# Kernel tuning notes

Measured on AMD Instinct MI355X. Metric: run time of the kernel, lower is better.

Reference implementation:

```python
import jax, jax.numpy as jnp
import numpy as np

B, T, D = 4, 2048, 1024
E, K, H = 8, 2, 2048

def setup_inputs() -> dict:
    key = jax.random.key(0)
    ks = jax.random.split(key, 5)
    scale = 0.02
    x = jax.random.normal(ks[0], (B, T, D), dtype=jnp.float32)
    gate_w = jax.random.normal(ks[1], (E, D), dtype=jnp.float32) * scale   # Linear(D->E) weight [out,in]
    w_gate = jax.random.normal(ks[2], (E, H, D), dtype=jnp.float32) * scale
    w_in = jax.random.normal(ks[3], (E, H, D), dtype=jnp.float32) * scale
    w_out = jax.random.normal(ks[4], (E, D, H), dtype=jnp.float32) * scale
    return {"x": x, "gate_w": gate_w, "w_gate": w_gate, "w_in": w_in, "w_out": w_out}

def reference(x, gate_w, w_gate, w_in, w_out):
    # Router: logits (B,T,E) -> top-k -> softmax over the k selected logits
    logits = jnp.einsum('btd,ed->bte', x, gate_w)
    topk_vals, topk_idx = jax.lax.top_k(logits, K)          # (B,T,K)
    routing = jax.nn.softmax(topk_vals, axis=-1)            # (B,T,K)

    out = jnp.zeros_like(x)
    # Masked-matmul: loop over the small fixed expert bank (E=8)
    for e in range(E):
        sel = (topk_idx == e)                               # (B,T,K) bool
        mask = sel.any(axis=-1)                             # (B,T)
        w = jnp.sum(routing * sel.astype(routing.dtype), axis=-1)  # (B,T)
        mx = x * mask[..., None].astype(x.dtype)            # (B,T,D)
        h = jax.nn.silu(jnp.einsum('btd,hd->bth', mx, w_gate[e])) * jnp.einsum('btd,hd->bth', mx, w_in[e])
        out = out + jnp.einsum('bth,dh->btd', h, w_out[e]) * w[..., None]
    return out
```

## Files before the change

kernel.cpp:

```cpp
#include <hip/hip_runtime.h>
#include <stdint.h>
#include <stddef.h>

#define NTOK 8192
#define DDIM 1024
#define NEXP 8
#define HDIM 2048
#define LSTRIDE (NTOK + 256)
#define NCHUNK 128
#define MAXROWS (2 * NTOK + NEXP * 256)

typedef __attribute__((ext_vector_type(4))) float f32x4;
typedef __attribute__((ext_vector_type(8))) short s16x8;
typedef __attribute__((ext_vector_type(4))) short s16x4;

static __device__ __forceinline__ unsigned short f2bf(float f) {
  union { float f; unsigned u; } v; v.f = f;
  unsigned r = v.u + 0x7FFFu + ((v.u >> 16) & 1u);
  return (unsigned short)(r >> 16);
}
static __device__ __forceinline__ float bf2f(unsigned short h) {
  union { unsigned u; float f; } v; v.u = ((unsigned)h) << 16;
  return v.f;
}

static __device__ __forceinline__ void gll16(const void* g, void* l) {
  __builtin_amdgcn_global_load_lds((const __attribute__((address_space(1))) void*)g,
                                   (__attribute__((address_space(3))) void*)l, 16, 0, 0);
}

#define BAR_MID() __builtin_amdgcn_s_barrier()
#define BAR_END() do { __builtin_amdgcn_s_barrier(); __builtin_amdgcn_sched_barrier(0); } while (0)
#define LGKM0() do { asm volatile("s_waitcnt lgkmcnt(0)" ::: "memory"); __builtin_amdgcn_sched_barrier(0); } while (0)
#define VMW6() asm volatile("s_waitcnt vmcnt(6)" ::: "memory")
#define VMW0() asm volatile("s_waitcnt vmcnt(0)" ::: "memory")

__global__ void k_sentinel(float* out) { if (threadIdx.x == 0) out[0] = 1.0e6f; }

__global__ __launch_bounds__(256) void k_prep(const float* __restrict__ x,
    const float* __restrict__ gw,
    const float* __restrict__ wgate, const float* __restrict__ win, const float* __restrict__ wout,
    unsigned short* __restrict__ wgb, unsigned short* __restrict__ wib, unsigned short* __restrict__ wob,
    unsigned* __restrict__ tokE, float2* __restrict__ tokW2, unsigned short* __restrict__ xbf) {
  int b = blockIdx.x;
  if (b >= 2048) {
    const float* srcs[3] = { wgate, win, wout };
    unsigned short* dsts[3] = { wgb, wib, wob };
    int g = (b - 2048) * 256 + threadIdx.x;
    const int stride = 1536 * 256;
#pragma unroll
    for (int it = 0; it < 16; ++it) {
      int arr = g >> 21;
      int idx = g & ((1 << 21) - 1);
      const f32x4* s = (const f32x4*)(srcs[arr] + (size_t)idx * 8);
      f32x4 a = s[0], c = s[1];
      s16x8 o;
      o[0] = f2bf(a[0]); o[1] = f2bf(a[1]); o[2] = f2bf(a[2]); o[3] = f2bf(a[3]);
      o[4] = f2bf(c[0]); o[5] = f2bf(c[1]); o[6] = f2bf(c[2]); o[7] = f2bf(c[3]);
      *(s16x8*)(dsts[arr] + (size_t)idx * 8) = o;
      g += stride;
    }
    return;
  }
  int lane = threadIdx.x & 63;
  int t = b * 4 + (threadIdx.x >> 6);
  const f32x4* x4 = (const f32x4*)x;
  const f32x4* g4 = (const f32x4*)gw;
  f32x4 xr[4];
#pragma unroll
  for (int j = 0; j < 4; ++j) xr[j] = x4[(size_t)t * 256 + j * 64 + lane];
#pragma unroll
  for (int j = 0; j < 4; ++j) {
    s16x4 o;
    o[0] = f2bf(xr[j][0]); o[1] = f2bf(xr[j][1]); o[2] = f2bf(xr[j][2]); o[3] = f2bf(xr[j][3]);
    *(s16x4*)(xbf + (size_t)t * DDIM + (j * 64 + lane) * 4) = o;
  }
  float le[8];
#pragma unroll
  for (int e = 0; e < 8; ++e) {
    float p = 0.f;
#pragma unroll
    for (int j = 0; j < 4; ++j) {
      f32x4 g = g4[e * 256 + j * 64 + lane];
      p += xr[j][0] * g[0] + xr[j][1] * g[1] + xr[j][2] * g[2] + xr[j][3] * g[3];
    }
#pragma unroll
    for (int off = 32; off > 0; off >>= 1) p += __shfl_xor(p, off, 64);
    le[e] = p;
  }
  if (lane == 0) {
    int i0 = 0; float v0 = le[0];
#pragma unroll
    for (int e = 1; e < 8; ++e) if (le[e] > v0) { v0 = le[e]; i0 = e; }
    int i1 = -1; float v1 = 0.f;
#pragma unroll
    for (int e = 0; e < 8; ++e) if (e != i0 && (i1 < 0 || le[e] > v1)) { v1 = le[e]; i1 = e; }
    float bb = __expf(v1 - v0);
    float s = 1.f + bb;
    tokE[t] = (unsigned)i0 | ((unsigned)i1 << 8);
    tokW2[t] = make_float2(1.f / s, bb / s);
  }
}

__global__ __launch_bounds__(64) void k_hist(const unsigned* __restrict__ tokE,
                                             int* __restrict__ cntTable) {
  __shared__ int c8[NEXP];
  int tid = threadIdx.x, c = blockIdx.x;
  if (tid < NEXP) c8[tid] = 0;
  __syncthreads();
  unsigned v = tokE[c * 64 + tid];
  atomicAdd(&c8[v & 255], 1);
  atomicAdd(&c8[(v >> 8) & 255], 1);
  __syncthreads();
  if (tid < NEXP) cntTable[tid * NCHUNK + c] = c8[tid];
}

__global__ __launch_bounds__(64) void k_scan(const int* __restrict__ cntTable,
                                             int* __restrict__ ctrl, int* __restrict__ cbL) {
  __shared__ int tot[NEXP];
  int e = threadIdx.x;
  if (e < NEXP) {
    int s = 0;
    for (int c = 0; c < NCHUNK; ++c) s += cntTable[e * NCHUNK + c];
    tot[e] = s; ctrl[e] = s;
  }
  __syncthreads();
  if (e == 0) {
    int acc = 0;
    for (int q = 0; q < NEXP; ++q) { ctrl[8 + q] = acc; acc += (tot[q] + 255) & ~255; }
  }
  if (e < NEXP) {
    int run = 0;
    for (int c = 0; c < NCHUNK; ++c) { cbL[e * NCHUNK + c] = run; run += cntTable[e * NCHUNK + c]; }
  }
}

__global__ __launch_bounds__(64) void k_scatter(const unsigned* __restrict__ tokE,
    const float2* __restrict__ tokW2, const int* __restrict__ cbL,
    int* __restrict__ listTok, float* __restrict__ listW, int* __restrict__ listSlot) {
  __shared__ int lcnt[NEXP];
  int tid = threadIdx.x, c = blockIdx.x;
  if (tid < NEXP) lcnt[tid] = 0;
  __syncthreads();
  int t = c * 64 + tid;
  unsigned v = tokE[t];
  int e0 = v & 255, e1 = (v >> 8) & 255;
  float2 w = tokW2[t];
  int l0 = atomicAdd(&lcnt[e0], 1);
  int l1 = atomicAdd(&lcnt[e1], 1);
  int i0 = cbL[e0 * NCHUNK + c] + l0;
  int i1 = cbL[e1 * NCHUNK + c] + l1;
  listTok[e0 * LSTRIDE + i0] = t; listW[e0 * LSTRIDE + i0] = w.x; listSlot[e0 * LSTRIDE + i0] = 0;
  listTok[e1 * LSTRIDE + i1] = t; listW[e1 * LSTRIDE + i1] = w.y; listSlot[e1 * LSTRIDE + i1] = 1;
}

__global__ __launch_bounds__(512, 2) void k_gemm1(const unsigned short* __restrict__ xbf,
    const unsigned short* __restrict__ wg, const unsigned short* __restrict__ wi,
    const int* __restrict__ ctrl, const int* __restrict__ listTok,
    unsigned short* __restrict__ hbuf) {
  int e = blockIdx.z;
  int cnt = ctrl[e];
  int m0 = blockIdx.y * 256;
  if (m0 >= cnt) return;
  int rowb = ctrl[8 + e];
  int n0 = blockIdx.x * 128;

  __shared__ __align__(16) char lds[131072];
  char* ldsc = &lds[0];

  int tid = threadIdx.x, lane = tid & 63, wv = tid >> 6;
  int wm = wv >> 1, wn = wv & 1;

  int srow = tid >> 3;
  int scol = (((tid & 7) ^ ((tid >> 3) & 7)) << 4);
  int sdst = wv << 10;
  const char* pA[2][2];
  const char* pBg[2];
  const char* pBi[2];
#pragma unroll
  for (int rg = 0; rg < 2; ++rg)
#pragma unroll
    for (int sb = 0; sb < 2; ++sb) {
      int tok = listTok[e * LSTRIDE + m0 + rg * 128 + sb * 64 + srow];
      pA[rg][sb] = (const char*)xbf + (size_t)tok * 2048 + scol;
    }
#pragma unroll
  for (int sb = 0; sb < 2; ++sb) {
    pBg[sb] = (const char*)wg + ((size_t)e * HDIM + n0 + sb * 64 + srow) * 2048 + scol;
    pBi[sb] = (const char*)wi + ((size_t)e * HDIM + n0 + sb * 64 + srow) * 2048 + scol;
  }

  int rowB = (lane & 15) << 7;
  int mk = (lane & 7) << 4;
  int q16 = (lane >> 4) << 4;
  int c0 = q16 ^ mk, c1 = (q16 + 64) ^ mk;
  int aO0 = 32768 + (wm >> 1) * 16384 + ((wm & 1) * 64) * 128 + rowB + c0;
  int aO1 = aO0 - c0 + c1;
  int gO0 = (wn * 64) * 128 + rowB + c0;
  int gO1 = gO0 - c0 + c1;
  int iO0 = 16384 + (wn * 64) * 128 + rowB + c0;
  int iO1 = iO0 - c0 + c1;

#define G1_STA(BUF, RG, KO) do { \
    gll16(pA[RG][0] + (KO), ldsc + (BUF) + 32768 + (RG) * 16384 + sdst); \
    gll16(pA[RG][1] + (KO), ldsc + (BUF) + 32768 + (RG) * 16384 + 8192 + sdst); } while (0)
#define G1_STG(BUF, KO) do { \
    gll16(pBg[0] + (KO), ldsc + (BUF) + sdst); \
    gll16(pBg[1] + (KO), ldsc + (BUF) + 8192 + sdst); } while (0)
#define G1_STI(BUF, KO) do { \
    gll16(pBi[0] + (KO), ldsc + (BUF) + 16384 + sdst); \
    gll16(pBi[1] + (KO), ldsc + (BUF) + 16384 + 8192 + sdst); } while (0)
#define G1_RDA(BUF) { _Pragma("unroll") for (int mf = 0; mf < 4; ++mf) { \
    af[mf][0] = *(const s16x8*)(ldsc + (BUF) + aO0 + mf * 2048); \
    af[mf][1] = *(const s16x8*)(ldsc + (BUF) + aO1 + mf * 2048); } }
#define G1_RDG(BUF) { _Pragma("unroll") for (int nf = 0; nf < 4; ++nf) { \
    bg[nf][0] = *(const s16x8*)(ldsc + (BUF) + gO0 + nf * 2048); \
    bg[nf][1] = *(const s16x8*)(ldsc + (BUF) + gO1 + nf * 2048); } }
#define G1_RDI(BUF) { _Pragma("unroll") for (int nf = 0; nf < 4; ++nf) { \
    bi[nf][0] = *(const s16x8*)(ldsc + (BUF) + iO0 + nf * 2048); \
    bi[nf][1] = *(const s16x8*)(ldsc + (BUF) + iO1 + nf * 2048); } }
#define G1_MMG(NH) do { __builtin_amdgcn_s_setprio(1); \
    _Pragma("unroll") for (int mf = 0; mf < 4; ++mf) _Pragma("unroll") for (int nf = 0; nf < 2; ++nf) { \
      accg[mf][(NH)*2+nf] = __builtin_amdgcn_mfma_f32_16x16x32_bf16(af[mf][0], bg[(NH)*2+nf][0], accg[mf][(NH)*2+nf], 0, 0, 0); \
      accg[mf][(NH)*2+nf] = __builtin_amdgcn_mfma_f32_16x16x32_bf16(af[mf][1], bg[(NH)*2+nf][1], accg[mf][(NH)*2+nf], 0, 0, 0); } \
    __builtin_amdgcn_s_setprio(0); } while (0)
#define G1_MMI(NH) do { __builtin_amdgcn_s_setprio(1); \
    _Pragma("unroll") for (int mf = 0; mf < 4; ++mf) _Pragma("unroll") for (int nf = 0; nf < 2; ++nf) { \
      acci[mf][(NH)*2+nf] = __builtin_amdgcn_mfma_f32_16x16x32_bf16(af[mf][0], bi[(NH)*2+nf][0], acci[mf][(NH)*2+nf], 0, 0, 0); \
      acci[mf][(NH)*2+nf] = __builtin_amdgcn_mfma_f32_16x16x32_bf16(af[mf][1], bi[(NH)*2+nf][1], acci[mf][(NH)*2+nf], 0, 0, 0); } \
    __builtin_amdgcn_s_setprio(0); } while (0)

  f32x4 accg[4][4], acci[4][4];
#pragma unroll
  for (int a = 0; a < 4; ++a)
#pragma unroll
    for (int b = 0; b < 4; ++b) { accg[a][b] = (f32x4){0.f,0.f,0.f,0.f}; acci[a][b] = (f32x4){0.f,0.f,0.f,0.f}; }
  s16x8 af[4][2], bg[4][2], bi[4][2];

  G1_STG(0, 0); G1_STA(0, 0, 0); G1_STI(0, 0); G1_STA(0, 1, 0);
  G1_STG(65536, 128); G1_STA(65536, 0, 128); G1_STI(65536, 128);
  VMW6();
  BAR_END();

  const int NIT = DDIM / 128;
  for (int i = 0; i < NIT; ++i) {
    const int koC = (2 * i + 1) * 128, koA = (2 * i + 2) * 128, koB = (2 * i + 3) * 128;
    const bool more = (i + 1 < NIT);
    G1_RDA(0); G1_RDG(0);
    G1_STA(65536, 1, koC);
    BAR_MID(); LGKM0();
    G1_MMG(0);
    BAR_END();
    if (more) G1_STG(0, koA);
    BAR_MID();
    G1_MMG(1);
    BAR_END();
    G1_RDI(0);
    if (more) G1_STA(0, 0, koA);
    BAR_MID(); LGKM0();
    G1_MMI(0);
    BAR_END();
    if (more) G1_STI(0, koA);
    BAR_MID();
    G1_MMI(1);
    if (more) VMW6(); else VMW0();
    BAR_END();
    G1_RDA(65536); G1_RDG(65536);
    if (more) G1_STA(0, 1, koA);
    BAR_MID(); LGKM0();
    G1_MMG(0);
    BAR_END();
    if (more) G1_STG(65536, koB);
    BAR_MID();
    G1_MMG(1);
    BAR_END();
    G1_RDI(65536);
    if (more) G1_STA(65536, 0, koB);
    BAR_MID(); LGKM0();
    G1_MMI(0);
    BAR_END();
    if (more) G1_STI(65536, koB);
    BAR_MID();
    G1_MMI(1);
    if (more) VMW6();
    BAR_END();
  }

#pragma unroll
  for (int mf = 0; mf < 4; ++mf)
#pragma unroll
    for (int j = 0; j < 4; ++j) {
      int r = wm * 64 + mf * 16 + ((lane >> 4) << 2) + j;
      size_t rowoff = (size_t)(rowb + m0 + r) * HDIM;
#pragma unroll
      for (int nf = 0; nf < 4; ++nf) {
        int cc = n0 + wn * 64 + nf * 16 + (lane & 15);
        float g = accg[mf][nf][j];
        float iv = acci[mf][nf][j];
        float hv = g / (1.f + __expf(-g)) * iv;
        hbuf[rowoff + cc] = f2bf(hv);
      }
    }
#undef G1_STA
#undef G1_STG
#undef G1_STI
#undef G1_RDA
#undef G1_RDG
#undef G1_RDI
#undef G1_MMG
#undef G1_MMI
}

__global__ __launch_bounds__(512, 2) void k_gemm2(const unsigned short* __restrict__ hbuf,
    const unsigned short* __restrict__ wo, const int* __restrict__ ctrl,
    const int* __restrict__ listTok, const float* __restrict__ listW,
    const int* __restrict__ listSlot, unsigned short* __restrict__ ybuf) {
  int e = blockIdx.z;
  int cnt = ctrl[e];
  int m0 = blockIdx.y * 256;
  if (m0 >= cnt) return;
  int rowb = ctrl[8 + e];
  int n0 = blockIdx.x * 128;

  __shared__ __align__(16) char lds[98304];
  char* ldsc = &lds[0];
#define BUF2 49152

  int tid = threadIdx.x, lane = tid & 63, wv = tid >> 6;
  int wm = wv >> 1, wn = wv & 1;

  int srow = tid >> 3;
  int scol = (((tid & 7) ^ ((tid >> 3) & 7)) << 4);
  int sdst = wv << 10;
  const char* pA[2][2];
  const char* pB[2];
#pragma unroll
  for (int rg = 0; rg < 2; ++rg)
#pragma unroll
    for (int sb = 0; sb < 2; ++sb)
      pA[rg][sb] = (const char*)hbuf + (size_t)(rowb + m0 + rg * 128 + sb * 64 + srow) * 4096 + scol;
#pragma unroll
  for (int sb = 0; sb < 2; ++sb)
    pB[sb] = (const char*)wo + ((size_t)e * DDIM + n0 + sb * 64 + srow) * 4096 + scol;

  int rowB = (lane & 15) << 7;
  int mk = (lane & 7) << 4;
  int q16 = (lane >> 4) << 4;
  int c0 = q16 ^ mk, c1 = (q16 + 64) ^ mk;
  int aO0 = wm * 8192 + rowB + c0;
  int aO1 = aO0 - c0 + c1;
  int bO0 = 32768 + wn * 8192 + rowB + c0;
  int bO1 = bO0 - c0 + c1;

#define G2_STA(BUF, RG, KO) do { \
    gll16(pA[RG][0] + (KO), ldsc + (BUF) + (RG) * 16384 + sdst); \
    gll16(pA[RG][1] + (KO), ldsc + (BUF) + (RG) * 16384 + 8192 + sdst); } while (0)
#define G2_STB(BUF, KO) do { \
    gll16(pB[0] + (KO), ldsc + (BUF) + 32768 + sdst); \
    gll16(pB[1] + (KO), ldsc + (BUF) + 32768 + 8192 + sdst); } while (0)
#define G2_RDA(BUF) { _Pragma("unroll") for (int mf = 0; mf < 4; ++mf) { \
    af[mf][0] = *(const s16x8*)(ldsc + (BUF) + aO0 + mf * 2048); \
    af[mf][1] = *(const s16x8*)(ldsc + (BUF) + aO1 + mf * 2048); } }
#define G2_RDB(BUF) { _Pragma("unroll") for (int nf = 0; nf < 4; ++nf) { \
    bf[nf][0] = *(const s16x8*)(ldsc + (BUF) + bO0 + nf * 2048); \
    bf[nf][1] = *(const s16x8*)(ldsc + (BUF) + bO1 + nf * 2048); } }
#define G2_MM(NH) do { __builtin_amdgcn_s_setprio(1); \
    _Pragma("unroll") for (int mf = 0; mf < 4; ++mf) _Pragma("unroll") for (int nf = 0; nf < 2; ++nf) { \
      acc[mf][(NH)*2+nf] = __builtin_amdgcn_mfma_f32_16x16x32_bf16(af[mf][0], bf[(NH)*2+nf][0], acc[mf][(NH)*2+nf], 0, 0, 0); \
      acc[mf][(NH)*2+nf] = __builtin_amdgcn_mfma_f32_16x16x32_bf16(af[mf][1], bf[(NH)*2+nf][1], acc[mf][(NH)*2+nf], 0, 0, 0); } \
    __builtin_amdgcn_s_setprio(0); } while (0)

  f32x4 acc[4][4];
#pragma unroll
  for (int a = 0; a < 4; ++a)
#pragma unroll
    for (int b = 0; b < 4; ++b) acc[a][b] = (f32x4){0.f,0.f,0.f,0.f};
  s16x8 af[4][2], bf[4][2];

  G2_STA(0, 0, 0); G2_STA(0, 1, 0); G2_STB(0, 0);
  G2_STA(BUF2, 0, 128); G2_STA(BUF2, 1, 128); G2_STB(BUF2, 128);
  VMW6();
  BAR_END();

  const int NIT = HDIM / 128;
  for (int i = 0; i < NIT; ++i) {
    const int koA = (2 * i + 2) * 128, koB = (2 * i + 3) * 128;
    const bool more = (i + 1 < NIT);
    G2_RDA(0); G2_RDB(0);
    BAR_MID(); LGKM0();
    G2_MM(0);
    BAR_END();
    if (more) { G2_STA(0, 0, koA); G2_STA(0, 1, koA); G2_STB(0, koA); }
    BAR_MID();
    G2_MM(1);
    if (more) VMW6(); else VMW0();
    BAR_END();
    G2_RDA(BUF2); G2_RDB(BUF2);
    BAR_MID(); LGKM0();
    G2_MM(0);
    BAR_END();
    if (more) { G2_STA(BUF2, 0, koB); G2_STA(BUF2, 1, koB); G2_STB(BUF2, koB); }
    BAR_MID();
    G2_MM(1);
    VMW6();
    BAR_END();
  }

#pragma unroll
  for (int mf = 0; mf < 4; ++mf)
#pragma unroll
    for (int j = 0; j < 4; ++j) {
      int r = wm * 64 + mf * 16 + ((lane >> 4) << 2) + j;
      int mrow = m0 + r;
      if (mrow < cnt) {
        int tok = listTok[e * LSTRIDE + mrow];
        float wgt = listW[e * LSTRIDE + mrow];
        int slot = listSlot[e * LSTRIDE + mrow];
        size_t base = ((size_t)slot * NTOK + tok) * DDIM + n0 + wn * 64;
#pragma unroll
        for (int nf = 0; nf < 4; ++nf)
          ybuf[base + nf * 16 + (lane & 15)] = f2bf(acc[mf][nf][j] * wgt);
      }
    }
#undef G2_STA
#undef G2_STB
#undef G2_RDA
#undef G2_RDB
#undef G2_MM
#undef BUF2
}

__global__ __launch_bounds__(256) void k_reduce(const unsigned short* __restrict__ ybuf,
                                                float* __restrict__ out, int n8) {
  int i = blockIdx.x * blockDim.x + threadIdx.x;
  int stride = gridDim.x * blockDim.x;
  const unsigned short* y0 = ybuf;
  const unsigned short* y1 = ybuf + (size_t)NTOK * DDIM;
  for (; i < n8; i += stride) {
    s16x8 a = *(const s16x8*)(y0 + (size_t)i * 8);
    s16x8 b = *(const s16x8*)(y1 + (size_t)i * 8);
    f32x4 o0, o1;
#pragma unroll
    for (int j = 0; j < 4; ++j) o0[j] = bf2f((unsigned short)a[j]) + bf2f((unsigned short)b[j]);
#pragma unroll
    for (int j = 0; j < 4; ++j) o1[j] = bf2f((unsigned short)a[4 + j]) + bf2f((unsigned short)b[4 + j]);
    f32x4* d = (f32x4*)(out + (size_t)i * 8);
    d[0] = o0; d[1] = o1;
  }
}

extern "C" void kernel_launch(void* const* d_in, const int* in_sizes, int n_in,
                              void* d_out, int out_size, void* d_ws, size_t ws_size,
                              hipStream_t stream) {
  const float* x     = (const float*)d_in[0];
  const float* gw    = (const float*)d_in[1];
  const float* wgate = (const float*)d_in[2];
  const float* win   = (const float*)d_in[3];
  const float* wout  = (const float*)d_in[4];
  float* out = (float*)d_out;

  const size_t LBYTES     = (size_t)NEXP * LSTRIDE * 4;
  const size_t OFF_LIST   = 256;
  const size_t OFF_LISTW  = OFF_LIST + LBYTES;
  const size_t ZERO_BYTES = OFF_LISTW;
  const size_t OFF_SLOT   = OFF_LISTW + LBYTES;
  const size_t OFF_CB     = OFF_SLOT + LBYTES;
  const size_t OFF_CT     = OFF_CB + 4096;
  const size_t OFF_TE     = OFF_CT + 4096;
  const size_t OFF_TW     = OFF_TE + (size_t)NTOK * 4;
  const size_t OFF_XBF = (size_t)1 << 20;
  const size_t OFF_WG  = OFF_XBF + (size_t)NTOK * DDIM * 2;
  const size_t OFF_WI  = OFF_WG + (size_t)NEXP * HDIM * DDIM * 2;
  const size_t OFF_WO  = OFF_WI + (size_t)NEXP * HDIM * DDIM * 2;
  const size_t OFF_H   = OFF_WO + (size_t)NEXP * DDIM * HDIM * 2;
  const size_t OFF_Y   = OFF_WG;
  const size_t TOTAL   = OFF_H + (size_t)MAXROWS * HDIM * 2;

  if (ws_size < TOTAL) { k_sentinel<<<1, 64, 0, stream>>>(out); return; }

  char* ws = (char*)d_ws;
  int* ctrl            = (int*)ws;
  int* listTok         = (int*)(ws + OFF_LIST);
  float* listW         = (float*)(ws + OFF_LISTW);
  int* listSlot        = (int*)(ws + OFF_SLOT);
  int* cbL             = (int*)(ws + OFF_CB);
  int* cntTable        = (int*)(ws + OFF_CT);
  unsigned* tokE       = (unsigned*)(ws + OFF_TE);
  float2* tokW2        = (float2*)(ws + OFF_TW);
  unsigned short* xbf  = (unsigned short*)(ws + OFF_XBF);
  unsigned short* wgb  = (unsigned short*)(ws + OFF_WG);
  unsigned short* wib  = (unsigned short*)(ws + OFF_WI);
  unsigned short* wob  = (unsigned short*)(ws + OFF_WO);
  unsigned short* hbuf = (unsigned short*)(ws + OFF_H);
  unsigned short* ybuf = (unsigned short*)(ws + OFF_Y);

  hipMemsetAsync(ws, 0, ZERO_BYTES, stream);

  k_prep<<<3584, 256, 0, stream>>>(x, gw, wgate, win, wout, wgb, wib, wob, tokE, tokW2, xbf);
  k_hist<<<NCHUNK, 64, 0, stream>>>(tokE, cntTable);
  k_scan<<<1, 64, 0, stream>>>(cntTable, ctrl, cbL);
  k_scatter<<<NCHUNK, 64, 0, stream>>>(tokE, tokW2, cbL, listTok, listW, listSlot);

  k_gemm1<<<dim3(HDIM / 128, NTOK / 256, NEXP), 512, 0, stream>>>(xbf, wgb, wib, ctrl, listTok, hbuf);
  k_gemm2<<<dim3(DDIM / 128, NTOK / 256, NEXP), 512, 0, stream>>>(hbuf, wob, ctrl, listTok, listW, listSlot, ybuf);
  k_reduce<<<512, 256, 0, stream>>>(ybuf, out, NTOK * DDIM / 8);
}
```

Measured before the change: 365.7 us.

## Overlap w_out bf16 conversion with gemm1 and merge histogram and scan kernels

Moves the fp32-to-bf16 conversion of w_out out of the prep kernel into an extra z-slice of gemm1 blocks, so it overlaps with the first expert GEMM instead of sitting on the critical path. Replaces the separate histogram and scan kernels with one kernel per expert that counts and prefix-sums chunk counts. Each GEMM block now recomputes the expert row base from the counts. The extra blocks compete with GEMM blocks for CUs and bandwidth.

```diff
diff --git a/kernel.cpp b/kernel.cpp
--- a/kernel.cpp
+++ b/kernel.cpp
@@ -37,17 +37,24 @@
 
 __global__ void k_sentinel(float* out) { if (threadIdx.x == 0) out[0] = 1.0e6f; }
 
+static __device__ __forceinline__ int rowbase(const int* __restrict__ ctrl, int e) {
+  int rowb = 0;
+#pragma unroll
+  for (int q = 0; q < NEXP; ++q) if (q < e) rowb += (ctrl[q] + 255) & ~255;
+  return rowb;
+}
+
 __global__ __launch_bounds__(256) void k_prep(const float* __restrict__ x,
     const float* __restrict__ gw,
-    const float* __restrict__ wgate, const float* __restrict__ win, const float* __restrict__ wout,
-    unsigned short* __restrict__ wgb, unsigned short* __restrict__ wib, unsigned short* __restrict__ wob,
+    const float* __restrict__ wgate, const float* __restrict__ win,
+    unsigned short* __restrict__ wgb, unsigned short* __restrict__ wib,
     unsigned* __restrict__ tokE, float2* __restrict__ tokW2, unsigned short* __restrict__ xbf) {
   int b = blockIdx.x;
   if (b >= 2048) {
-    const float* srcs[3] = { wgate, win, wout };
-    unsigned short* dsts[3] = { wgb, wib, wob };
+    const float* srcs[2] = { wgate, win };
+    unsigned short* dsts[2] = { wgb, wib };
     int g = (b - 2048) * 256 + threadIdx.x;
-    const int stride = 1536 * 256;
+    const int stride = 1024 * 256;
 #pragma unroll
     for (int it = 0; it < 16; ++it) {
       int arr = g >> 21;
@@ -102,36 +109,23 @@
   }
 }
 
-__global__ __launch_bounds__(64) void k_hist(const unsigned* __restrict__ tokE,
-                                             int* __restrict__ cntTable) {
-  __shared__ int c8[NEXP];
-  int tid = threadIdx.x, c = blockIdx.x;
-  if (tid < NEXP) c8[tid] = 0;
+__global__ __launch_bounds__(128) void k_histscan(const unsigned* __restrict__ tokE,
+                                                  int* __restrict__ ctrl, int* __restrict__ cbL) {
+  __shared__ int cnts[NCHUNK];
+  int e = blockIdx.x, c = threadIdx.x;
+  int n = 0;
+  const unsigned* p = tokE + c * 64;
+#pragma unroll 8
+  for (int i = 0; i < 64; ++i) {
+    unsigned v = p[i];
+    n += ((int)(v & 255) == e) + ((int)((v >> 8) & 255) == e);
+  }
+  cnts[c] = n;
   __syncthreads();
-  unsigned v = tokE[c * 64 + tid];
-  atomicAdd(&c8[v & 255], 1);
-  atomicAdd(&c8[(v >> 8) & 255], 1);
-  __syncthreads();
-  if (tid < NEXP) cntTable[tid * NCHUNK + c] = c8[tid];
-}
-
-__global__ __launch_bounds__(64) void k_scan(const int* __restrict__ cntTable,
-                                             int* __restrict__ ctrl, int* __restrict__ cbL) {
-  __shared__ int tot[NEXP];
-  int e = threadIdx.x;
-  if (e < NEXP) {
-    int s = 0;
-    for (int c = 0; c < NCHUNK; ++c) s += cntTable[e * NCHUNK + c];
-    tot[e] = s; ctrl[e] = s;
-  }
-  __syncthreads();
-  if (e == 0) {
-    int acc = 0;
-    for (int q = 0; q < NEXP; ++q) { ctrl[8 + q] = acc; acc += (tot[q] + 255) & ~255; }
-  }
-  if (e < NEXP) {
+  if (c == 0) {
     int run = 0;
-    for (int c = 0; c < NCHUNK; ++c) { cbL[e * NCHUNK + c] = run; run += cntTable[e * NCHUNK + c]; }
+    for (int q = 0; q < NCHUNK; ++q) { int t = cnts[q]; cbL[e * NCHUNK + q] = run; run += t; }
+    ctrl[e] = run;
   }
 }
 
@@ -157,12 +151,28 @@
 __global__ __launch_bounds__(512, 2) void k_gemm1(const unsigned short* __restrict__ xbf,
     const unsigned short* __restrict__ wg, const unsigned short* __restrict__ wi,
     const int* __restrict__ ctrl, const int* __restrict__ listTok,
-    unsigned short* __restrict__ hbuf) {
+    unsigned short* __restrict__ hbuf,
+    const float* __restrict__ wout, unsigned short* __restrict__ wob) {
   int e = blockIdx.z;
+  if (e == 8) {
+    int g = (blockIdx.x + blockIdx.y * 16) * 512 + threadIdx.x;
+    const int stride = 512 * 512;
+#pragma unroll
+    for (int it = 0; it < 8; ++it) {
+      const f32x4* s = (const f32x4*)(wout + (size_t)g * 8);
+      f32x4 a = s[0], c = s[1];
+      s16x8 o;
+      o[0] = f2bf(a[0]); o[1] = f2bf(a[1]); o[2] = f2bf(a[2]); o[3] = f2bf(a[3]);
+      o[4] = f2bf(c[0]); o[5] = f2bf(c[1]); o[6] = f2bf(c[2]); o[7] = f2bf(c[3]);
+      *(s16x8*)(wob + (size_t)g * 8) = o;
+      g += stride;
+    }
+    return;
+  }
   int cnt = ctrl[e];
   int m0 = blockIdx.y * 256;
   if (m0 >= cnt) return;
-  int rowb = ctrl[8 + e];
+  int rowb = rowbase(ctrl, e);
   int n0 = blockIdx.x * 128;
 
   __shared__ __align__(16) char lds[131072];
@@ -319,7 +329,7 @@
   int cnt = ctrl[e];
   int m0 = blockIdx.y * 256;
   if (m0 >= cnt) return;
-  int rowb = ctrl[8 + e];
+  int rowb = rowbase(ctrl, e);
   int n0 = blockIdx.x * 128;
 
   __shared__ __align__(16) char lds[98304];
@@ -465,8 +475,7 @@
   const size_t ZERO_BYTES = OFF_LISTW;
   const size_t OFF_SLOT   = OFF_LISTW + LBYTES;
   const size_t OFF_CB     = OFF_SLOT + LBYTES;
-  const size_t OFF_CT     = OFF_CB + 4096;
-  const size_t OFF_TE     = OFF_CT + 4096;
+  const size_t OFF_TE     = OFF_CB + 4096;
   const size_t OFF_TW     = OFF_TE + (size_t)NTOK * 4;
   const size_t OFF_XBF = (size_t)1 << 20;
   const size_t OFF_WG  = OFF_XBF + (size_t)NTOK * DDIM * 2;
@@ -484,7 +493,6 @@
   float* listW         = (float*)(ws + OFF_LISTW);
   int* listSlot        = (int*)(ws + OFF_SLOT);
   int* cbL             = (int*)(ws + OFF_CB);
-  int* cntTable        = (int*)(ws + OFF_CT);
   unsigned* tokE       = (unsigned*)(ws + OFF_TE);
   float2* tokW2        = (float2*)(ws + OFF_TW);
   unsigned short* xbf  = (unsigned short*)(ws + OFF_XBF);
@@ -496,12 +504,11 @@
 
   hipMemsetAsync(ws, 0, ZERO_BYTES, stream);
 
-  k_prep<<<3584, 256, 0, stream>>>(x, gw, wgate, win, wout, wgb, wib, wob, tokE, tokW2, xbf);
-  k_hist<<<NCHUNK, 64, 0, stream>>>(tokE, cntTable);
-  k_scan<<<1, 64, 0, stream>>>(cntTable, ctrl, cbL);
+  k_prep<<<3072, 256, 0, stream>>>(x, gw, wgate, win, wgb, wib, tokE, tokW2, xbf);
+  k_histscan<<<NEXP, 128, 0, stream>>>(tokE, ctrl, cbL);
   k_scatter<<<NCHUNK, 64, 0, stream>>>(tokE, tokW2, cbL, listTok, listW, listSlot);
 
-  k_gemm1<<<dim3(HDIM / 128, NTOK / 256, NEXP), 512, 0, stream>>>(xbf, wgb, wib, ctrl, listTok, hbuf);
+  k_gemm1<<<dim3(HDIM / 128, NTOK / 256, NEXP + 1), 512, 0, stream>>>(xbf, wgb, wib, ctrl, listTok, hbuf, wout, wob);
   k_gemm2<<<dim3(DDIM / 128, NTOK / 256, NEXP), 512, 0, stream>>>(hbuf, wob, ctrl, listTok, listW, listSlot, ybuf);
   k_reduce<<<512, 256, 0, stream>>>(ybuf, out, NTOK * DDIM / 8);
 }
```

Result: faster. 354.2 us (-3.2%).
